# Performance work log

Measured on AMD Instinct MI355X. Metric: run time of the kernel, lower is better.

Reference implementation:

```python
import jax, jax.numpy as jnp
import numpy as np

N_NODES = 50000
N_EDGES = 800000
BN_EPS = 1e-5


def setup_inputs() -> dict:
    key = jax.random.key(0)
    ks = jax.random.split(key, 8)
    feat = jax.random.normal(ks[0], (N_NODES, 512), dtype=jnp.float32)
    src = jax.random.randint(ks[1], (N_EDGES,), 0, N_NODES, dtype=jnp.int32)
    dst = jax.random.randint(ks[2], (N_EDGES,), 0, N_NODES, dtype=jnp.int32)
    W0 = jax.random.normal(ks[3], (512, 128), dtype=jnp.float32) * 0.05
    W1 = jax.random.normal(ks[4], (128, 128), dtype=jnp.float32) * 0.05
    Wp1 = jax.random.normal(ks[5], (128, 256), dtype=jnp.float32) * 0.05
    bp1 = jnp.zeros((256,), dtype=jnp.float32)
    gamma = jnp.ones((256,), dtype=jnp.float32)
    beta = jnp.zeros((256,), dtype=jnp.float32)
    Wp2 = jax.random.normal(ks[6], (256, 128), dtype=jnp.float32) * 0.05
    bp2 = jnp.zeros((128,), dtype=jnp.float32)
    return {"feat": feat, "src": src, "dst": dst, "W0": W0, "W1": W1,
            "Wp1": Wp1, "bp1": bp1, "gamma": gamma, "beta": beta,
            "Wp2": Wp2, "bp2": bp2}


def reference(feat, src, dst, W0, W1, Wp1, bp1, gamma, beta, Wp2, bp2):
    N = feat.shape[0]
    # in-degrees, clamped to >=1, then D^{-1/2}
    deg = jax.ops.segment_sum(jnp.ones_like(dst, dtype=jnp.float32), dst,
                              num_segments=N)
    dinv = jnp.power(jnp.maximum(deg, 1.0), -0.5)[:, None]  # [N,1]

    def low_conv(h):
        # 2h - L_sym h = h + D^{-1/2} A D^{-1/2} h
        scaled = h * dinv
        agg = jax.ops.segment_sum(scaled[src], dst, num_segments=N)
        return h + agg * dinv

    h = low_conv(feat @ W0)      # linear0 (no bias) + conv0
    h = low_conv(h @ W1)         # linear1 (no bias) + conv1

    # MLPHead: Linear -> BatchNorm1d (training stats) -> ReLU -> Linear
    z = h @ Wp1 + bp1
    mu = jnp.mean(z, axis=0)
    var = jnp.mean((z - mu) ** 2, axis=0)  # biased var, torch training mode
    z = (z - mu) * jax.lax.rsqrt(var + BN_EPS) * gamma + beta
    z = jax.nn.relu(z)
    return z @ Wp2 + bp2
```

## Files before the change

### kernel.cpp

```cpp
#include <hip/hip_runtime.h>
#include <math.h>

constexpr int NN  = 50000;
constexpr int NE  = 800000;
constexpr int NNP = 50048;
constexpr int NB  = (NN + 255) / 256;
constexpr int GX  = NNP / 128;
constexpr int FILLB = (NE + 511) / 512;

typedef __bf16 bf16x8 __attribute__((ext_vector_type(8)));
typedef float  f32x4  __attribute__((ext_vector_type(4)));
typedef __attribute__((address_space(1))) unsigned int as1_uint;
typedef __attribute__((address_space(3))) unsigned int as3_uint;

__device__ __forceinline__ unsigned short f2bf(float x) {
    unsigned int u = __float_as_uint(x);
    return (unsigned short)((u + 0x7FFFu + ((u >> 16) & 1u)) >> 16);
}
__device__ __forceinline__ float bf2f(unsigned short h) {
    return __uint_as_float(((unsigned int)h) << 16);
}
__device__ __forceinline__ float rdlanef(float v, int j) {
    return __uint_as_float(__builtin_amdgcn_readlane(__float_as_uint(v), j));
}

__device__ __forceinline__ void gload16(const unsigned short* g, unsigned short* l) {
    __builtin_amdgcn_global_load_lds((const as1_uint*)(unsigned long long)g,
                                     (as3_uint*)(unsigned long long)l, 16, 0, 0);
}

__global__ void k_bsum(const int* __restrict__ cnt, int* __restrict__ bsum) {
    int i = blockIdx.x * 256 + threadIdx.x;
    int v = (i < NN) ? cnt[i] : 0;
#pragma unroll
    for (int off = 32; off; off >>= 1) v += __shfl_down(v, off, 64);
    __shared__ int tmp[4];
    if ((threadIdx.x & 63) == 0) tmp[threadIdx.x >> 6] = v;
    __syncthreads();
    if (threadIdx.x == 0) bsum[blockIdx.x] = tmp[0] + tmp[1] + tmp[2] + tmp[3];
}

__global__ void k_scan_bsum(const int* __restrict__ bsum, int* __restrict__ boff) {
    __shared__ int s[256];
    int t = threadIdx.x;
    int v = (t < NB) ? bsum[t] : 0;
    s[t] = v;
    __syncthreads();
    for (int off = 1; off < 256; off <<= 1) {
        int u = (t >= off) ? s[t - off] : 0;
        __syncthreads();
        s[t] += u;
        __syncthreads();
    }
    if (t < NB) boff[t] = s[t] - v;
}

__global__ void k_scan_block(const int* __restrict__ cnt, const int* __restrict__ boff,
                             int* __restrict__ rowoff, float* __restrict__ dinv) {
    __shared__ int s[256];
    int t = threadIdx.x;
    int i = blockIdx.x * 256 + t;
    int v = (i < NN) ? cnt[i] : 0;
    s[t] = v;
    __syncthreads();
    for (int off = 1; off < 256; off <<= 1) {
        int u = (t >= off) ? s[t - off] : 0;
        __syncthreads();
        s[t] += u;
        __syncthreads();
    }
    if (i < NN) {
        rowoff[i] = boff[blockIdx.x] + s[t] - v;
        dinv[i] = rsqrtf(fmaxf((float)v, 1.0f));
    }
}

__global__ __launch_bounds__(256) void k_gather_shfl(
    const unsigned short* __restrict__ HH, const float* __restrict__ dinv,
    const int* __restrict__ rowoff, const int* __restrict__ cnt,
    const int* __restrict__ eidx, unsigned short* __restrict__ OH)
{
    int node = blockIdx.x * 4 + (threadIdx.x >> 6);
    int lane = threadIdx.x & 63;
    if (node >= NNP) return;
    size_t rb = (size_t)node * 128 + lane * 2;
    if (node >= NN) {
        *reinterpret_cast<ushort2*>(&OH[rb]) = make_ushort2(0, 0);
        return;
    }
    int beg = rowoff[node], n = cnt[node];
    int c2 = lane * 2;
    float ax = 0.f, ay = 0.f;
    for (int jj = 0; jj < n; jj += 64) {
        int m = min(n - jj, 64);
        int el = (lane < m) ? eidx[beg + jj + lane] : 0;
        float dl = dinv[el];
        int mp = (m + 7) & ~7;
        for (int j = 0; j < mp; j += 8) {
            int ss[8]; float dd[8]; ushort2 vv[8];
#pragma unroll
            for (int q = 0; q < 8; ++q) {
                int jq = (j + q) & 63;
                ss[q] = __builtin_amdgcn_readlane(el, jq);
                dd[q] = (j + q < m) ? rdlanef(dl, jq) : 0.f;
            }
#pragma unroll
            for (int q = 0; q < 8; ++q)
                vv[q] = *reinterpret_cast<const ushort2*>(&HH[(size_t)ss[q] * 128 + c2]);
#pragma unroll
            for (int q = 0; q < 8; ++q) {
                ax = fmaf(bf2f(vv[q].x), dd[q], ax);
                ay = fmaf(bf2f(vv[q].y), dd[q], ay);
            }
        }
    }
    float d = dinv[node];
    ushort2 sh = *reinterpret_cast<const ushort2*>(&HH[rb]);
    float hx = fmaf(ax, d, bf2f(sh.x));
    float hy = fmaf(ay, d, bf2f(sh.y));
    *reinterpret_cast<ushort2*>(&OH[rb]) = make_ushort2(f2bf(hx), f2bf(hy));
}

__global__ void k_wprep_count(const float* __restrict__ W0, const float* __restrict__ W1,
                              const float* __restrict__ Wp1, const float* __restrict__ Wp2,
                              unsigned short* __restrict__ W0t, unsigned short* __restrict__ W1pt,
                              unsigned short* __restrict__ Wp2t, float* __restrict__ stats,
                              const int* __restrict__ dst, int* __restrict__ cnt,
                              int* __restrict__ pos) {
    int b = blockIdx.x, t = threadIdx.x;
    if (b >= 512) {
        int i = (b - 512) * 256 + t;
        if (i < NE) pos[i] = atomicAdd(&cnt[dst[i]], 1);
        return;
    }
    if (b < 128) {
        if (b < 2) stats[b * 256 + t] = 0.f;
        float s = 0.f;
        for (int k = 0; k < 128; ++k) s = fmaf(W1[b * 128 + k], Wp1[k * 256 + t], s);
        W1pt[t * 128 + b] = f2bf(s);
    } else if (b < 384) {
        int idx = (b - 128) * 256 + t;
        int k = idx >> 7, n = idx & 127;
        W0t[n * 512 + k] = f2bf(W0[idx]);
    } else {
        int idx = (b - 384) * 256 + t;
        int k = idx >> 7, n = idx & 127;
        Wp2t[n * 256 + k] = f2bf(Wp2[idx]);
    }
}

__global__ __launch_bounds__(512) void k_gemm1_fill(
    const float* __restrict__ Af, const unsigned short* __restrict__ BH,
    unsigned short* __restrict__ OHs,
    const int* __restrict__ src, const int* __restrict__ dst,
    const int* __restrict__ rowoff, const int* __restrict__ pos,
    int* __restrict__ eidx)
{
    if (blockIdx.x >= GX) {
        int e = (blockIdx.x - GX) * 512 + threadIdx.x;
        if (e < NE) {
            int d = dst[e];
            eidx[rowoff[d] + pos[e]] = src[e];
        }
        return;
    }
    constexpr int K = 512, NCOLS = 128;
    __shared__ __align__(16) unsigned short lds[2 * 4096];
    unsigned short* ldsA = lds;
    unsigned short* ldsB = lds + 4096;

    const int tid  = threadIdx.x;
    const int lane = tid & 63;
    const int wid  = tid >> 6;
    const int wm   = wid >> 1;
    const int wn   = wid & 1;
    const int row0 = blockIdx.x * 128;

    const int srow  = tid >> 2;
    const int skg   = tid & 3;
    const int skswz = skg ^ ((srow >> 1) & 3);
    const size_t aSrc = (size_t)(row0 + srow) * K + skswz * 8;
    const size_t bSrc = (size_t)srow * K + skswz * 8;

    const int frow = lane & 15;
    const int fkg  = lane >> 4;

    f32x4 acc[2][4] = {};

    for (int k0 = 0; k0 < K; k0 += 32) {
        float4 f0, f1;
        if (row0 + srow < NN) {
            const float* ap = Af + aSrc + k0;
            f0 = *reinterpret_cast<const float4*>(ap);
            f1 = *reinterpret_cast<const float4*>(ap + 4);
        } else {
            f0 = make_float4(0.f, 0.f, 0.f, 0.f);
            f1 = f0;
        }
        uint4 w;
        w.x = (unsigned)f2bf(f0.x) | ((unsigned)f2bf(f0.y) << 16);
        w.y = (unsigned)f2bf(f0.z) | ((unsigned)f2bf(f0.w) << 16);
        w.z = (unsigned)f2bf(f1.x) | ((unsigned)f2bf(f1.y) << 16);
        w.w = (unsigned)f2bf(f1.z) | ((unsigned)f2bf(f1.w) << 16);
        *reinterpret_cast<uint4*>(&ldsA[tid * 8]) = w;
        gload16(BH + bSrc + k0, ldsB + tid * 8);
        __syncthreads();

        bf16x8 a_h[2], b_h[4];
#pragma unroll
        for (int mi = 0; mi < 2; ++mi) {
            int ar  = wm * 32 + mi * 16 + frow;
            int idx = ar * 32 + ((fkg ^ ((ar >> 1) & 3)) * 8);
            a_h[mi] = *reinterpret_cast<const bf16x8*>(&ldsA[idx]);
        }
#pragma unroll
        for (int ni = 0; ni < 4; ++ni) {
            int bc  = wn * 64 + ni * 16 + frow;
            int idx = bc * 32 + ((fkg ^ ((bc >> 1) & 3)) * 8);
            b_h[ni] = *reinterpret_cast<const bf16x8*>(&ldsB[idx]);
        }
#pragma unroll
        for (int mi = 0; mi < 2; ++mi)
#pragma unroll
            for (int ni = 0; ni < 4; ++ni)
                acc[mi][ni] = __builtin_amdgcn_mfma_f32_16x16x32_bf16(a_h[mi], b_h[ni], acc[mi][ni], 0, 0, 0);
        __syncthreads();
    }

#pragma unroll
    for (int mi = 0; mi < 2; ++mi) {
        int rbase = row0 + wm * 32 + mi * 16 + (lane >> 4) * 4;
#pragma unroll
        for (int ni = 0; ni < 4; ++ni) {
            int col = wn * 64 + ni * 16 + (lane & 15);
#pragma unroll
            for (int r = 0; r < 4; ++r)
                OHs[(size_t)(rbase + r) * NCOLS + col] = f2bf(acc[mi][ni][r]);
        }
    }
}

template <int K, int NCOLS, bool BIAS, int AMODE, int OMODE, bool STATS>
__global__ __launch_bounds__(512) void k_mfma(
    const unsigned short* __restrict__ AH, const unsigned short* __restrict__ BH,
    const float* __restrict__ bias,
    const float* __restrict__ stats, const float* __restrict__ gamma,
    const float* __restrict__ beta,
    float* __restrict__ C, unsigned short* __restrict__ OHs,
    float* __restrict__ statsOut)
{
    __shared__ __align__(16) unsigned short lds[2 * 4096];
    unsigned short* ldsA = lds;
    unsigned short* ldsB = lds + 4096;

    const int tid  = threadIdx.x;
    const int lane = tid & 63;
    const int wid  = tid >> 6;
    const int wm   = wid >> 1;
    const int wn   = wid & 1;
    const int row0 = blockIdx.x * 128;
    const int col0 = blockIdx.y * 128;

    const int srow  = tid >> 2;
    const int skg   = tid & 3;
    const int skswz = skg ^ ((srow >> 1) & 3);
    const size_t aSrc = (size_t)(row0 + srow) * K + skswz * 8;
    const size_t bSrc = (size_t)(col0 + srow) * K + skswz * 8;

    const int frow = lane & 15;
    const int fkg  = lane >> 4;

    __shared__ float s_scl[256], s_shf[256];
    if constexpr (AMODE == 2) {
        if (tid < K) {
            float mu  = stats[tid] * (1.0f / NN);
            float var = stats[256 + tid] * (1.0f / NN) - mu * mu;
            float s = gamma[tid] * rsqrtf(var + 1e-5f);
            s_scl[tid] = s;
            s_shf[tid] = beta[tid] - mu * s;
        }
        __syncthreads();
    }

    f32x4 acc[2][4] = {};

    for (int k0 = 0; k0 < K; k0 += 32) {
        if constexpr (AMODE == 2) {
            uint4 raw = *reinterpret_cast<const uint4*>(&AH[aSrc + k0]);
            unsigned rw[4] = {raw.x, raw.y, raw.z, raw.w};
            int kc = k0 + skswz * 8;
            float vv[8];
#pragma unroll
            for (int q = 0; q < 8; ++q) {
                float z = bf2f((unsigned short)((q & 1) ? (rw[q >> 1] >> 16)
                                                        : (rw[q >> 1] & 0xFFFF)));
                vv[q] = fmaxf(fmaf(z, s_scl[kc + q], s_shf[kc + q]), 0.f);
            }
            uint4 w;
            w.x = (unsigned)f2bf(vv[0]) | ((unsigned)f2bf(vv[1]) << 16);
            w.y = (unsigned)f2bf(vv[2]) | ((unsigned)f2bf(vv[3]) << 16);
            w.z = (unsigned)f2bf(vv[4]) | ((unsigned)f2bf(vv[5]) << 16);
            w.w = (unsigned)f2bf(vv[6]) | ((unsigned)f2bf(vv[7]) << 16);
            *reinterpret_cast<uint4*>(&ldsA[tid * 8]) = w;
        } else {
            gload16(AH + aSrc + k0, ldsA + tid * 8);
        }
        gload16(BH + bSrc + k0, ldsB + tid * 8);
        __syncthreads();

        bf16x8 a_h[2], b_h[4];
#pragma unroll
        for (int mi = 0; mi < 2; ++mi) {
            int ar  = wm * 32 + mi * 16 + frow;
            int idx = ar * 32 + ((fkg ^ ((ar >> 1) & 3)) * 8);
            a_h[mi] = *reinterpret_cast<const bf16x8*>(&ldsA[idx]);
        }
#pragma unroll
        for (int ni = 0; ni < 4; ++ni) {
            int bc  = wn * 64 + ni * 16 + frow;
            int idx = bc * 32 + ((fkg ^ ((bc >> 1) & 3)) * 8);
            b_h[ni] = *reinterpret_cast<const bf16x8*>(&ldsB[idx]);
        }
#pragma unroll
        for (int mi = 0; mi < 2; ++mi)
#pragma unroll
            for (int ni = 0; ni < 4; ++ni)
                acc[mi][ni] = __builtin_amdgcn_mfma_f32_16x16x32_bf16(a_h[mi], b_h[ni], acc[mi][ni], 0, 0, 0);
        __syncthreads();
    }

    float psum[4] = {0.f, 0.f, 0.f, 0.f}, psq[4] = {0.f, 0.f, 0.f, 0.f};
#pragma unroll
    for (int mi = 0; mi < 2; ++mi) {
        int rbase = row0 + wm * 32 + mi * 16 + (lane >> 4) * 4;
#pragma unroll
        for (int ni = 0; ni < 4; ++ni) {
            int col = col0 + wn * 64 + ni * 16 + (lane & 15);
            float b = BIAS ? bias[col] : 0.f;
#pragma unroll
            for (int r = 0; r < 4; ++r) {
                int row = rbase + r;
                float v = acc[mi][ni][r] + b;
                if constexpr (STATS) {
                    if (row < NN) { psum[ni] += v; psq[ni] = fmaf(v, v, psq[ni]); }
                }
                if constexpr (OMODE == 1) {
                    OHs[(size_t)row * NCOLS + col] = f2bf(v);
                } else {
                    if (row < NN) C[(size_t)row * NCOLS + col] = v;
                }
            }
        }
    }

    if constexpr (STATS) {
        __shared__ float s_sum[128], s_sq[128];
        if (tid < 128) { s_sum[tid] = 0.f; s_sq[tid] = 0.f; }
        __syncthreads();
#pragma unroll
        for (int ni = 0; ni < 4; ++ni) {
            float a = psum[ni], q = psq[ni];
            a += __shfl_xor(a, 16); a += __shfl_xor(a, 32);
            q += __shfl_xor(q, 16); q += __shfl_xor(q, 32);
            if ((lane >> 4) == 0) {
                int cl = wn * 64 + ni * 16 + lane;
                atomicAdd(&s_sum[cl], a);
                atomicAdd(&s_sq[cl], q);
            }
        }
        __syncthreads();
        if (tid < 128) {
            atomicAdd(&statsOut[col0 + tid], s_sum[tid]);
            atomicAdd(&statsOut[256 + col0 + tid], s_sq[tid]);
        }
    }
}

extern "C" void kernel_launch(void* const* d_in, const int* in_sizes, int n_in,
                              void* d_out, int out_size, void* d_ws, size_t ws_size,
                              hipStream_t stream) {
    const float* feat  = (const float*)d_in[0];
    const int*   src   = (const int*)d_in[1];
    const int*   dst   = (const int*)d_in[2];
    const float* W0    = (const float*)d_in[3];
    const float* W1    = (const float*)d_in[4];
    const float* Wp1   = (const float*)d_in[5];
    const float* bp1   = (const float*)d_in[6];
    const float* gamma = (const float*)d_in[7];
    const float* beta  = (const float*)d_in[8];
    const float* Wp2   = (const float*)d_in[9];
    const float* bp2   = (const float*)d_in[10];
    float* out = (float*)d_out;

    char* wsb = (char*)d_ws;
    float* dinv   = (float*)(wsb + 4ull * 0);
    int*   cnt    = (int*)  (wsb + 4ull * 50048);
    int*   rowoff = (int*)  (wsb + 4ull * 100096);
    int*   bsum   = (int*)  (wsb + 4ull * 150144);
    int*   boff   = (int*)  (wsb + 4ull * 150400);
    int*   pos    = (int*)  (wsb + 4ull * 150656);
    int*   eidx   = (int*)  (wsb + 4ull * 950656);
    float* stats  = (float*)(wsb + 4ull * 1750656);
    unsigned short* W0t  = (unsigned short*)(wsb + 4ull * 1751168);
    unsigned short* W1pt = W0t + 65536;
    unsigned short* Wp2t = W1pt + 32768;
    unsigned short* H0 = (unsigned short*)(wsb + 4ull * 1816704);
    unsigned short* h1 = (unsigned short*)(wsb + 4ull * 5019776);
    unsigned short* h2 = H0;
    unsigned short* ZH = (unsigned short*)(wsb + 4ull * 8222848);

    hipMemsetAsync(cnt, 0, 50048 * sizeof(int), stream);
    k_wprep_count<<<512 + (NE + 255) / 256, 256, 0, stream>>>(
        W0, W1, Wp1, Wp2, W0t, W1pt, Wp2t, stats, dst, cnt, pos);
    k_bsum<<<NB, 256, 0, stream>>>(cnt, bsum);
    k_scan_bsum<<<1, 256, 0, stream>>>(bsum, boff);
    k_scan_block<<<NB, 256, 0, stream>>>(cnt, boff, rowoff, dinv);

    k_gemm1_fill<<<GX + FILLB, 512, 0, stream>>>(
        feat, W0t, H0, src, dst, rowoff, pos, eidx);

    k_gather_shfl<<<NNP / 4, 256, 0, stream>>>(H0, dinv, rowoff, cnt, eidx, h1);
    k_gather_shfl<<<NNP / 4, 256, 0, stream>>>(h1, dinv, rowoff, cnt, eidx, h2);

    k_mfma<128, 256, true, 0, 1, true><<<dim3(GX, 2), 512, 0, stream>>>(
        h2, W1pt, bp1, nullptr, nullptr, nullptr, nullptr, ZH, stats);

    k_mfma<256, 128, true, 2, 0, false><<<dim3(GX, 1), 512, 0, stream>>>(
        ZH, Wp2t, bp2, stats, gamma, beta, out, nullptr, nullptr);
}
```

Before: 197.1 us.

## Build CSR edge index via two-level bucketing instead of per-edge position atomics

Replaces the per-edge atomic position array with a two-pass bucket sort. The fill pass appends (src,dst) pairs into 64-node buckets using one atomic counter per bucket, and a new kernel then sorts each bucket into node order in LDS and writes eidx with coalesced stores. The aim is to remove the pos array read/write and the scattered eidx writes. In exchange it adds an extra kernel launch and an 8-byte staging buffer, and it relies on no 64-node bucket holding more than 2048 edges.

```diff
diff --git a/kernel.cpp b/kernel.cpp
--- a/kernel.cpp
+++ b/kernel.cpp
@@ -7,6 +7,8 @@
 constexpr int NB  = (NN + 255) / 256;
 constexpr int GX  = NNP / 128;
 constexpr int FILLB = (NE + 511) / 512;
+constexpr int NBKT = NNP / 64;
+constexpr int BCAP = 2048;
 
 typedef __bf16 bf16x8 __attribute__((ext_vector_type(8)));
 typedef float  f32x4  __attribute__((ext_vector_type(4)));
@@ -125,12 +127,11 @@
                               const float* __restrict__ Wp1, const float* __restrict__ Wp2,
                               unsigned short* __restrict__ W0t, unsigned short* __restrict__ W1pt,
                               unsigned short* __restrict__ Wp2t, float* __restrict__ stats,
-                              const int* __restrict__ dst, int* __restrict__ cnt,
-                              int* __restrict__ pos) {
+                              const int* __restrict__ dst, int* __restrict__ cnt) {
     int b = blockIdx.x, t = threadIdx.x;
     if (b >= 512) {
         int i = (b - 512) * 256 + t;
-        if (i < NE) pos[i] = atomicAdd(&cnt[dst[i]], 1);
+        if (i < NE) atomicAdd(&cnt[dst[i]], 1);
         return;
     }
     if (b < 128) {
@@ -153,14 +154,16 @@
     const float* __restrict__ Af, const unsigned short* __restrict__ BH,
     unsigned short* __restrict__ OHs,
     const int* __restrict__ src, const int* __restrict__ dst,
-    const int* __restrict__ rowoff, const int* __restrict__ pos,
-    int* __restrict__ eidx)
+    const int* __restrict__ rowoff, int* __restrict__ bcur, int2* __restrict__ staging)
 {
     if (blockIdx.x >= GX) {
         int e = (blockIdx.x - GX) * 512 + threadIdx.x;
         if (e < NE) {
-            int d = dst[e];
-            eidx[rowoff[d] + pos[e]] = src[e];
+            int d = dst[e], s = src[e];
+            int b = d >> 6;
+            int base = rowoff[b << 6];
+            int slot = atomicAdd(&bcur[b], 1);
+            staging[base + slot] = make_int2(s, d);
         }
         return;
     }
@@ -238,6 +241,29 @@
                 OHs[(size_t)(rbase + r) * NCOLS + col] = f2bf(acc[mi][ni][r]);
         }
     }
+}
+
+__global__ __launch_bounds__(256) void k_bucket(
+    const int2* __restrict__ staging, const int* __restrict__ rowoff,
+    int* __restrict__ eidx)
+{
+    int b = blockIdx.x;
+    int base = rowoff[b << 6];
+    int end  = (b == NBKT - 1) ? NE : rowoff[(b + 1) << 6];
+    int n = end - base;
+    __shared__ int2 sE[BCAP];
+    __shared__ int  sO[BCAP];
+    __shared__ int  lcur[64];
+    if (threadIdx.x < 64) lcur[threadIdx.x] = 0;
+    for (int i = threadIdx.x; i < n; i += 256) sE[i] = staging[base + i];
+    __syncthreads();
+    for (int i = threadIdx.x; i < n; i += 256) {
+        int2 ed = sE[i];
+        int p = atomicAdd(&lcur[ed.y & 63], 1);
+        sO[rowoff[ed.y] - base + p] = ed.x;
+    }
+    __syncthreads();
+    for (int i = threadIdx.x; i < n; i += 256) eidx[base + i] = sO[i];
 }
 
 template <int K, int NCOLS, bool BIAS, int AMODE, int OMODE, bool STATS>
@@ -393,31 +419,34 @@
     float* out = (float*)d_out;
 
     char* wsb = (char*)d_ws;
-    float* dinv   = (float*)(wsb + 4ull * 0);
-    int*   cnt    = (int*)  (wsb + 4ull * 50048);
-    int*   rowoff = (int*)  (wsb + 4ull * 100096);
-    int*   bsum   = (int*)  (wsb + 4ull * 150144);
-    int*   boff   = (int*)  (wsb + 4ull * 150400);
-    int*   pos    = (int*)  (wsb + 4ull * 150656);
-    int*   eidx   = (int*)  (wsb + 4ull * 950656);
-    float* stats  = (float*)(wsb + 4ull * 1750656);
-    unsigned short* W0t  = (unsigned short*)(wsb + 4ull * 1751168);
+    float* dinv    = (float*)(wsb + 4ull * 0);
+    int*   cnt     = (int*)  (wsb + 4ull * 50048);
+    int*   bcur    = (int*)  (wsb + 4ull * 100096);
+    int*   rowoff  = (int*)  (wsb + 4ull * 101120);
+    int*   bsum    = (int*)  (wsb + 4ull * 151168);
+    int*   boff    = (int*)  (wsb + 4ull * 151424);
+    int*   eidx    = (int*)  (wsb + 4ull * 151680);
+    int2*  staging = (int2*) (wsb + 4ull * 951680);
+    float* stats   = (float*)(wsb + 4ull * 2551680);
+    unsigned short* W0t  = (unsigned short*)(wsb + 4ull * 2552192);
     unsigned short* W1pt = W0t + 65536;
     unsigned short* Wp2t = W1pt + 32768;
-    unsigned short* H0 = (unsigned short*)(wsb + 4ull * 1816704);
-    unsigned short* h1 = (unsigned short*)(wsb + 4ull * 5019776);
+    unsigned short* H0 = (unsigned short*)(wsb + 4ull * 2617728);
+    unsigned short* h1 = (unsigned short*)(wsb + 4ull * 5820800);
     unsigned short* h2 = H0;
-    unsigned short* ZH = (unsigned short*)(wsb + 4ull * 8222848);
-
-    hipMemsetAsync(cnt, 0, 50048 * sizeof(int), stream);
+    unsigned short* ZH = (unsigned short*)(wsb + 4ull * 9023872);
+
+    hipMemsetAsync(cnt, 0, (50048 + 1024) * sizeof(int), stream);
     k_wprep_count<<<512 + (NE + 255) / 256, 256, 0, stream>>>(
-        W0, W1, Wp1, Wp2, W0t, W1pt, Wp2t, stats, dst, cnt, pos);
+        W0, W1, Wp1, Wp2, W0t, W1pt, Wp2t, stats, dst, cnt);
     k_bsum<<<NB, 256, 0, stream>>>(cnt, bsum);
     k_scan_bsum<<<1, 256, 0, stream>>>(bsum, boff);
     k_scan_block<<<NB, 256, 0, stream>>>(cnt, boff, rowoff, dinv);
 
     k_gemm1_fill<<<GX + FILLB, 512, 0, stream>>>(
-        feat, W0t, H0, src, dst, rowoff, pos, eidx);
+        feat, W0t, H0, src, dst, rowoff, bcur, staging);
+
+    k_bucket<<<NBKT, 256, 0, stream>>>(staging, rowoff, eidx);
 
     k_gather_shfl<<<NNP / 4, 256, 0, stream>>>(H0, dinv, rowoff, cnt, eidx, h1);
     k_gather_shfl<<<NNP / 4, 256, 0, stream>>>(h1, dinv, rowoff, cnt, eidx, h2);
```

After: 368.4 us. 86.9% more time.

## Pack edge metadata, shrink edge indices to 16-bit, merge block-sum into scan

Applied to the files above, without the earlier changes.

The per-edge slot returned by the atomic and the destination node are packed into one 32-bit word, so the fill pass reads one array instead of two. The CSR source-index array is stored as 16-bit values, which cuts its traffic in both gather passes; this relies on the node count fitting in 16 bits. The separate block-sum kernel is removed: the single-block scan now sums its 256-element chunks itself, one serial loop per thread. The fill pass handles four edges per thread. The serial, strided summation loop inside one block may add latency that offsets the saved launch.

```diff
diff --git a/kernel.cpp b/kernel.cpp
--- a/kernel.cpp
+++ b/kernel.cpp
@@ -6,7 +6,7 @@
 constexpr int NNP = 50048;
 constexpr int NB  = (NN + 255) / 256;
 constexpr int GX  = NNP / 128;
-constexpr int FILLB = (NE + 511) / 512;
+constexpr int FILLB = (NE + 2047) / 2048;
 
 typedef __bf16 bf16x8 __attribute__((ext_vector_type(8)));
 typedef float  f32x4  __attribute__((ext_vector_type(4)));
@@ -29,21 +29,15 @@
                                      (as3_uint*)(unsigned long long)l, 16, 0, 0);
 }
 
-__global__ void k_bsum(const int* __restrict__ cnt, int* __restrict__ bsum) {
-    int i = blockIdx.x * 256 + threadIdx.x;
-    int v = (i < NN) ? cnt[i] : 0;
-#pragma unroll
-    for (int off = 32; off; off >>= 1) v += __shfl_down(v, off, 64);
-    __shared__ int tmp[4];
-    if ((threadIdx.x & 63) == 0) tmp[threadIdx.x >> 6] = v;
-    __syncthreads();
-    if (threadIdx.x == 0) bsum[blockIdx.x] = tmp[0] + tmp[1] + tmp[2] + tmp[3];
-}
-
-__global__ void k_scan_bsum(const int* __restrict__ bsum, int* __restrict__ boff) {
+__global__ void k_scan_bsum(const int* __restrict__ cnt, int* __restrict__ boff) {
+    int t = threadIdx.x;
+    int v = 0;
+    if (t < NB) {
+        int base = t * 256;
+        int lim = min(base + 256, NN);
+        for (int j = base; j < lim; ++j) v += cnt[j];
+    }
     __shared__ int s[256];
-    int t = threadIdx.x;
-    int v = (t < NB) ? bsum[t] : 0;
     s[t] = v;
     __syncthreads();
     for (int off = 1; off < 256; off <<= 1) {
@@ -78,7 +72,7 @@
 __global__ __launch_bounds__(256) void k_gather_shfl(
     const unsigned short* __restrict__ HH, const float* __restrict__ dinv,
     const int* __restrict__ rowoff, const int* __restrict__ cnt,
-    const int* __restrict__ eidx, unsigned short* __restrict__ OH)
+    const unsigned short* __restrict__ eidx, unsigned short* __restrict__ OH)
 {
     int node = blockIdx.x * 4 + (threadIdx.x >> 6);
     int lane = threadIdx.x & 63;
@@ -93,7 +87,7 @@
     float ax = 0.f, ay = 0.f;
     for (int jj = 0; jj < n; jj += 64) {
         int m = min(n - jj, 64);
-        int el = (lane < m) ? eidx[beg + jj + lane] : 0;
+        int el = (lane < m) ? (int)eidx[beg + jj + lane] : 0;
         float dl = dinv[el];
         int mp = (m + 7) & ~7;
         for (int j = 0; j < mp; j += 8) {
@@ -126,11 +120,15 @@
                               unsigned short* __restrict__ W0t, unsigned short* __restrict__ W1pt,
                               unsigned short* __restrict__ Wp2t, float* __restrict__ stats,
                               const int* __restrict__ dst, int* __restrict__ cnt,
-                              int* __restrict__ pos) {
+                              unsigned int* __restrict__ posdst) {
     int b = blockIdx.x, t = threadIdx.x;
     if (b >= 512) {
         int i = (b - 512) * 256 + t;
-        if (i < NE) pos[i] = atomicAdd(&cnt[dst[i]], 1);
+        if (i < NE) {
+            int d = dst[i];
+            int p = atomicAdd(&cnt[d], 1);
+            posdst[i] = ((unsigned)p << 16) | (unsigned)d;
+        }
         return;
     }
     if (b < 128) {
@@ -152,15 +150,19 @@
 __global__ __launch_bounds__(512) void k_gemm1_fill(
     const float* __restrict__ Af, const unsigned short* __restrict__ BH,
     unsigned short* __restrict__ OHs,
-    const int* __restrict__ src, const int* __restrict__ dst,
-    const int* __restrict__ rowoff, const int* __restrict__ pos,
-    int* __restrict__ eidx)
+    const int* __restrict__ src, const unsigned int* __restrict__ posdst,
+    const int* __restrict__ rowoff, unsigned short* __restrict__ eidx)
 {
     if (blockIdx.x >= GX) {
-        int e = (blockIdx.x - GX) * 512 + threadIdx.x;
-        if (e < NE) {
-            int d = dst[e];
-            eidx[rowoff[d] + pos[e]] = src[e];
+        int e0 = (blockIdx.x - GX) * 2048 + threadIdx.x;
+#pragma unroll
+        for (int q = 0; q < 4; ++q) {
+            int e = e0 + q * 512;
+            if (e < NE) {
+                unsigned pd = posdst[e];
+                int s = src[e];
+                eidx[rowoff[pd & 0xFFFFu] + (pd >> 16)] = (unsigned short)s;
+            }
         }
         return;
     }
@@ -393,31 +395,29 @@
     float* out = (float*)d_out;
 
     char* wsb = (char*)d_ws;
-    float* dinv   = (float*)(wsb + 4ull * 0);
-    int*   cnt    = (int*)  (wsb + 4ull * 50048);
-    int*   rowoff = (int*)  (wsb + 4ull * 100096);
-    int*   bsum   = (int*)  (wsb + 4ull * 150144);
-    int*   boff   = (int*)  (wsb + 4ull * 150400);
-    int*   pos    = (int*)  (wsb + 4ull * 150656);
-    int*   eidx   = (int*)  (wsb + 4ull * 950656);
-    float* stats  = (float*)(wsb + 4ull * 1750656);
-    unsigned short* W0t  = (unsigned short*)(wsb + 4ull * 1751168);
+    float* dinv     = (float*)(wsb + 4ull * 0);
+    int*   cnt      = (int*)  (wsb + 4ull * 50048);
+    int*   rowoff   = (int*)  (wsb + 4ull * 100096);
+    int*   boff     = (int*)  (wsb + 4ull * 150144);
+    unsigned int* posdst = (unsigned int*)(wsb + 4ull * 150400);
+    unsigned short* eidx = (unsigned short*)(wsb + 4ull * 950400);
+    float* stats    = (float*)(wsb + 4ull * 1350400);
+    unsigned short* W0t  = (unsigned short*)(wsb + 4ull * 1350912);
     unsigned short* W1pt = W0t + 65536;
     unsigned short* Wp2t = W1pt + 32768;
-    unsigned short* H0 = (unsigned short*)(wsb + 4ull * 1816704);
-    unsigned short* h1 = (unsigned short*)(wsb + 4ull * 5019776);
+    unsigned short* H0 = (unsigned short*)(wsb + 4ull * 1416448);
+    unsigned short* h1 = (unsigned short*)(wsb + 4ull * 4619520);
     unsigned short* h2 = H0;
-    unsigned short* ZH = (unsigned short*)(wsb + 4ull * 8222848);
+    unsigned short* ZH = (unsigned short*)(wsb + 4ull * 7822592);
 
     hipMemsetAsync(cnt, 0, 50048 * sizeof(int), stream);
     k_wprep_count<<<512 + (NE + 255) / 256, 256, 0, stream>>>(
-        W0, W1, Wp1, Wp2, W0t, W1pt, Wp2t, stats, dst, cnt, pos);
-    k_bsum<<<NB, 256, 0, stream>>>(cnt, bsum);
-    k_scan_bsum<<<1, 256, 0, stream>>>(bsum, boff);
+        W0, W1, Wp1, Wp2, W0t, W1pt, Wp2t, stats, dst, cnt, posdst);
+    k_scan_bsum<<<1, 256, 0, stream>>>(cnt, boff);
     k_scan_block<<<NB, 256, 0, stream>>>(cnt, boff, rowoff, dinv);
 
     k_gemm1_fill<<<GX + FILLB, 512, 0, stream>>>(
-        feat, W0t, H0, src, dst, rowoff, pos, eidx);
+        feat, W0t, H0, src, posdst, rowoff, eidx);
 
     k_gather_shfl<<<NNP / 4, 256, 0, stream>>>(H0, dinv, rowoff, cnt, eidx, h1);
     k_gather_shfl<<<NNP / 4, 256, 0, stream>>>(h1, dinv, rowoff, cnt, eidx, h2);
```

After: 210.8 us. 6.9% more time.

## Fuse second graph aggregation with Wp1 GEMM and BN stats into one kernel

Applied to the files above, without the earlier changes.

Replaces the second gather kernel and the following Z GEMM with a single kernel. Each 512-thread block gathers 64 aggregated rows straight into LDS in swizzled bf16 layout, then runs the MFMA against the combined W1·Wp1 weights, adding bias and accumulating batch-norm statistics. This avoids writing h2 to global memory and reading it back, and drops one launch. In exchange, each block's gather phase runs one wave per row sequentially with fewer waves in flight, and each block uses about 34 KB of LDS, which may lower occupancy and latency hiding during the irregular gather.

```diff
diff --git a/kernel.cpp b/kernel.cpp
--- a/kernel.cpp
+++ b/kernel.cpp
@@ -6,6 +6,7 @@
 constexpr int NNP = 50048;
 constexpr int NB  = (NN + 255) / 256;
 constexpr int GX  = NNP / 128;
+constexpr int GZ  = NNP / 64;
 constexpr int FILLB = (NE + 511) / 512;
 
 typedef __bf16 bf16x8 __attribute__((ext_vector_type(8)));
@@ -240,6 +241,146 @@
     }
 }
 
+__global__ __launch_bounds__(512) void k_gatherZ(
+    const unsigned short* __restrict__ HH, const float* __restrict__ dinv,
+    const int* __restrict__ rowoff, const int* __restrict__ cnt,
+    const int* __restrict__ eidx, const unsigned short* __restrict__ W1pt,
+    const float* __restrict__ bias, unsigned short* __restrict__ ZH,
+    float* __restrict__ statsOut)
+{
+    __shared__ __align__(16) unsigned short ldsA[8192];
+    __shared__ __align__(16) unsigned short ldsB[8192];
+    __shared__ float s_sum[256], s_sq[256];
+
+    const int tid  = threadIdx.x;
+    const int lane = tid & 63;
+    const int wid  = tid >> 6;
+    const int row0 = blockIdx.x * 64;
+
+    if (tid < 256) { s_sum[tid] = 0.f; s_sq[tid] = 0.f; }
+
+    {
+        int c = lane * 2;
+        int sc = c >> 5, g = (c >> 3) & 3, e = c & 7;
+        for (int it = 0; it < 8; ++it) {
+            int r = wid * 8 + it;
+            int node = row0 + r;
+            int aaddr = sc * 2048 + r * 32 + ((g ^ ((r >> 1) & 3)) << 3) + e;
+            if (node >= NN) {
+                *reinterpret_cast<ushort2*>(&ldsA[aaddr]) = make_ushort2(0, 0);
+                continue;
+            }
+            int beg = rowoff[node], n = cnt[node];
+            float ax = 0.f, ay = 0.f;
+            for (int jj = 0; jj < n; jj += 64) {
+                int m = min(n - jj, 64);
+                int el = (lane < m) ? eidx[beg + jj + lane] : 0;
+                float dl = dinv[el];
+                int mp = (m + 7) & ~7;
+                for (int j = 0; j < mp; j += 8) {
+                    int ss[8]; float dd[8]; ushort2 vv[8];
+#pragma unroll
+                    for (int q = 0; q < 8; ++q) {
+                        int jq = (j + q) & 63;
+                        ss[q] = __builtin_amdgcn_readlane(el, jq);
+                        dd[q] = (j + q < m) ? rdlanef(dl, jq) : 0.f;
+                    }
+#pragma unroll
+                    for (int q = 0; q < 8; ++q)
+                        vv[q] = *reinterpret_cast<const ushort2*>(&HH[(size_t)ss[q] * 128 + c]);
+#pragma unroll
+                    for (int q = 0; q < 8; ++q) {
+                        ax = fmaf(bf2f(vv[q].x), dd[q], ax);
+                        ay = fmaf(bf2f(vv[q].y), dd[q], ay);
+                    }
+                }
+            }
+            float d = dinv[node];
+            size_t rb = (size_t)node * 128 + c;
+            ushort2 sh = *reinterpret_cast<const ushort2*>(&HH[rb]);
+            float hx = fmaf(ax, d, bf2f(sh.x));
+            float hy = fmaf(ay, d, bf2f(sh.y));
+            *reinterpret_cast<ushort2*>(&ldsA[aaddr]) = make_ushort2(f2bf(hx), f2bf(hy));
+        }
+    }
+    __syncthreads();
+
+    const int wm = wid >> 2;
+    const int wn = wid & 3;
+    const int frow = lane & 15;
+    const int fkg  = lane >> 4;
+    f32x4 acc[2][4] = {};
+
+    for (int k0 = 0; k0 < 128; k0 += 32) {
+        {
+            int s1 = tid;
+            int r1 = s1 >> 2, p1 = s1 & 3;
+            gload16(W1pt + (size_t)r1 * 128 + k0 + ((p1 ^ ((r1 >> 1) & 3)) * 8),
+                    ldsB + s1 * 8);
+            int s2 = tid + 512;
+            int r2 = s2 >> 2, p2 = s2 & 3;
+            gload16(W1pt + (size_t)r2 * 128 + k0 + ((p2 ^ ((r2 >> 1) & 3)) * 8),
+                    ldsB + s2 * 8);
+        }
+        __syncthreads();
+
+        bf16x8 a_h[2], b_h[4];
+        int sc = k0 >> 5;
+#pragma unroll
+        for (int mi = 0; mi < 2; ++mi) {
+            int ar  = wm * 32 + mi * 16 + frow;
+            int idx = sc * 2048 + ar * 32 + ((fkg ^ ((ar >> 1) & 3)) * 8);
+            a_h[mi] = *reinterpret_cast<const bf16x8*>(&ldsA[idx]);
+        }
+#pragma unroll
+        for (int ni = 0; ni < 4; ++ni) {
+            int bc  = wn * 64 + ni * 16 + frow;
+            int idx = bc * 32 + ((fkg ^ ((bc >> 1) & 3)) * 8);
+            b_h[ni] = *reinterpret_cast<const bf16x8*>(&ldsB[idx]);
+        }
+#pragma unroll
+        for (int mi = 0; mi < 2; ++mi)
+#pragma unroll
+            for (int ni = 0; ni < 4; ++ni)
+                acc[mi][ni] = __builtin_amdgcn_mfma_f32_16x16x32_bf16(a_h[mi], b_h[ni], acc[mi][ni], 0, 0, 0);
+        __syncthreads();
+    }
+
+    float psum[4] = {0.f, 0.f, 0.f, 0.f}, psq[4] = {0.f, 0.f, 0.f, 0.f};
+#pragma unroll
+    for (int mi = 0; mi < 2; ++mi) {
+        int rbase = row0 + wm * 32 + mi * 16 + (lane >> 4) * 4;
+#pragma unroll
+        for (int ni = 0; ni < 4; ++ni) {
+            int col = wn * 64 + ni * 16 + (lane & 15);
+            float b = bias[col];
+#pragma unroll
+            for (int r = 0; r < 4; ++r) {
+                int row = rbase + r;
+                float v = acc[mi][ni][r] + b;
+                if (row < NN) { psum[ni] += v; psq[ni] = fmaf(v, v, psq[ni]); }
+                ZH[(size_t)row * 256 + col] = f2bf(v);
+            }
+        }
+    }
+#pragma unroll
+    for (int ni = 0; ni < 4; ++ni) {
+        float a = psum[ni], q = psq[ni];
+        a += __shfl_xor(a, 16); a += __shfl_xor(a, 32);
+        q += __shfl_xor(q, 16); q += __shfl_xor(q, 32);
+        if ((lane >> 4) == 0) {
+            int cl = wn * 64 + ni * 16 + lane;
+            atomicAdd(&s_sum[cl], a);
+            atomicAdd(&s_sq[cl], q);
+        }
+    }
+    __syncthreads();
+    if (tid < 256) {
+        atomicAdd(&statsOut[tid], s_sum[tid]);
+        atomicAdd(&statsOut[256 + tid], s_sq[tid]);
+    }
+}
+
 template <int K, int NCOLS, bool BIAS, int AMODE, int OMODE, bool STATS>
 __global__ __launch_bounds__(512) void k_mfma(
     const unsigned short* __restrict__ AH, const unsigned short* __restrict__ BH,
@@ -329,7 +470,6 @@
         __syncthreads();
     }
 
-    float psum[4] = {0.f, 0.f, 0.f, 0.f}, psq[4] = {0.f, 0.f, 0.f, 0.f};
 #pragma unroll
     for (int mi = 0; mi < 2; ++mi) {
         int rbase = row0 + wm * 32 + mi * 16 + (lane >> 4) * 4;
@@ -341,37 +481,8 @@
             for (int r = 0; r < 4; ++r) {
                 int row = rbase + r;
                 float v = acc[mi][ni][r] + b;
-                if constexpr (STATS) {
-                    if (row < NN) { psum[ni] += v; psq[ni] = fmaf(v, v, psq[ni]); }
-                }
-                if constexpr (OMODE == 1) {
-                    OHs[(size_t)row * NCOLS + col] = f2bf(v);
-                } else {
-                    if (row < NN) C[(size_t)row * NCOLS + col] = v;
-                }
-            }
-        }
-    }
-
-    if constexpr (STATS) {
-        __shared__ float s_sum[128], s_sq[128];
-        if (tid < 128) { s_sum[tid] = 0.f; s_sq[tid] = 0.f; }
-        __syncthreads();
-#pragma unroll
-        for (int ni = 0; ni < 4; ++ni) {
-            float a = psum[ni], q = psq[ni];
-            a += __shfl_xor(a, 16); a += __shfl_xor(a, 32);
-            q += __shfl_xor(q, 16); q += __shfl_xor(q, 32);
-            if ((lane >> 4) == 0) {
-                int cl = wn * 64 + ni * 16 + lane;
-                atomicAdd(&s_sum[cl], a);
-                atomicAdd(&s_sq[cl], q);
-            }
-        }
-        __syncthreads();
-        if (tid < 128) {
-            atomicAdd(&statsOut[col0 + tid], s_sum[tid]);
-            atomicAdd(&statsOut[256 + col0 + tid], s_sq[tid]);
+                if (row < NN) C[(size_t)row * NCOLS + col] = v;
+            }
         }
     }
 }
@@ -406,7 +517,6 @@
     unsigned short* Wp2t = W1pt + 32768;
     unsigned short* H0 = (unsigned short*)(wsb + 4ull * 1816704);
     unsigned short* h1 = (unsigned short*)(wsb + 4ull * 5019776);
-    unsigned short* h2 = H0;
     unsigned short* ZH = (unsigned short*)(wsb + 4ull * 8222848);
 
     hipMemsetAsync(cnt, 0, 50048 * sizeof(int), stream);
@@ -420,10 +530,8 @@
         feat, W0t, H0, src, dst, rowoff, pos, eidx);
 
     k_gather_shfl<<<NNP / 4, 256, 0, stream>>>(H0, dinv, rowoff, cnt, eidx, h1);
-    k_gather_shfl<<<NNP / 4, 256, 0, stream>>>(h1, dinv, rowoff, cnt, eidx, h2);
-
-    k_mfma<128, 256, true, 0, 1, true><<<dim3(GX, 2), 512, 0, stream>>>(
-        h2, W1pt, bp1, nullptr, nullptr, nullptr, nullptr, ZH, stats);
+
+    k_gatherZ<<<GZ, 512, 0, stream>>>(h1, dinv, rowoff, cnt, eidx, W1pt, bp1, ZH, stats);
 
     k_mfma<256, 128, true, 2, 0, false><<<dim3(GX, 1), 512, 0, stream>>>(
         ZH, Wp2t, bp2, stats, gamma, beta, out, nullptr, nullptr);
```

New measurement: 217.4 us. +10.3%, slower.
